# Performance work log

Measured on AMD Instinct MI355X. Metric: run time of the kernel, lower is better.

Reference implementation:

```python
import jax, jax.numpy as jnp
import numpy as np

DIM = 768
NUM_HEADS = 12
DECAY_RATE = 5.0


def setup_inputs() -> dict:
    key = jax.random.key(0)
    k1, k2, k3, k4 = jax.random.split(key, 4)
    B, N, C = 4, 1024, DIM
    x = jax.random.normal(k1, (B, N, C), dtype=jnp.float32)
    # torch nn.Linear weights: y = x @ W.T ; qkv_bias=False
    qkv_w = jax.random.normal(k2, (3 * C, C), dtype=jnp.float32) * (1.0 / np.sqrt(C))
    proj_w = jax.random.normal(k3, (C, C), dtype=jnp.float32) * (1.0 / np.sqrt(C))
    proj_b = jax.random.normal(k4, (C,), dtype=jnp.float32) * 0.01
    return {"x": x, "qkv_w": qkv_w, "proj_w": proj_w, "proj_b": proj_b, "cur_epoch": 3}


def reference(x, qkv_w, proj_w, proj_b, cur_epoch):
    B, N, C = x.shape
    H = NUM_HEADS
    hd = C // H
    scale = hd ** -0.5

    qkv = (x @ qkv_w.T).reshape(B, N, 3, H, hd).transpose(2, 0, 3, 1, 4)  # [3,B,H,N,hd]
    q, k, v = qkv[0], qkv[1], qkv[2]

    scores = jnp.einsum("bhqd,bhkd->bhqk", q, k) * scale
    logp = jax.nn.log_softmax(scores, axis=-1)
    attn = jnp.exp(logp)  # [B,H,N,N]

    # Per-key entropy: column j of attn flattened over (B,H,N) is renormalized
    # by Categorical; dividing by num_heads cancels under normalization.
    # H(p/s) = log(s) - (1/s) * sum(p * log p)
    s = jnp.sum(attn, axis=(0, 1, 2))                 # [N]
    plogp = jnp.sum(attn * logp, axis=(0, 1, 2))      # [N]
    entropies = jnp.log(s) - plogp / s

    # threshold decay: factor = sum_{i=0}^{cur_epoch-1} decay*exp(-(i+1))
    factor = DECAY_RATE * float(np.sum(np.exp(-(np.arange(cur_epoch) + 1.0))))
    entropy_threshold = float(np.log(C)) - factor

    # attn[:,:,:,keep] @ v[:,:,keep,:] == (attn * mask) @ v  (zeroed columns drop out)
    mask = (entropies <= entropy_threshold).astype(attn.dtype)  # [N]
    out = jnp.einsum("bhqk,bhkd->bhqd", attn * mask[None, None, None, :], v)
    out = out.transpose(0, 2, 1, 3).reshape(B, N, C)
    out = out @ proj_w.T + proj_b
    return out
```

## Files before the change

### kernel.cpp

```cpp
#include <hip/hip_runtime.h>


typedef __bf16 bf16x8 __attribute__((ext_vector_type(8)));
typedef __bf16 bf16x4 __attribute__((ext_vector_type(4)));
typedef float  f32x4  __attribute__((ext_vector_type(4)));

#define MFMA16(a, b, c) __builtin_amdgcn_mfma_f32_16x16x32_bf16((a), (b), (c), 0, 0, 0)

__global__ __launch_bounds__(256) void kc_conv(
    const float* __restrict__ x, const float* __restrict__ qw, const float* __restrict__ pw,
    __bf16* __restrict__ xb, __bf16* __restrict__ qwb, __bf16* __restrict__ pwb,
    float* __restrict__ colSP, int* __restrict__ keepCnt)
{
  const int i = blockIdx.x * 256 + threadIdx.x;
  const float4* src;
  __bf16* dst;
  int j;
  if (i < 786432)       { src = (const float4*)x;  dst = xb;  j = i; }
  else if (i < 1228800) { src = (const float4*)qw; dst = qwb; j = i - 786432; }
  else                  { src = (const float4*)pw; dst = pwb; j = i - 1228800; }
  const float4 f = src[j];
  bf16x4 o;
  o[0] = (__bf16)f.x; o[1] = (__bf16)f.y; o[2] = (__bf16)f.z; o[3] = (__bf16)f.w;
  *(bf16x4*)(dst + 4 * (size_t)j) = o;
  if (i < 2048) colSP[i] = 0.f;
  if (i == 0) *keepCnt = 0;
}

__global__ __launch_bounds__(256) void kg_qkv(
    const __bf16* __restrict__ A, const __bf16* __restrict__ Bm,
    __bf16* __restrict__ qb, __bf16* __restrict__ kb, float* __restrict__ v)
{
  __shared__ __bf16 As[64 * 72];
  __shared__ __bf16 Bs[64 * 72];
  const int tid = threadIdx.x;
  const int w = tid >> 6, lane = tid & 63, quad = lane >> 4, l = lane & 15;
  const int r0 = blockIdx.y * 64, c0 = blockIdx.x * 64;
  const int row = tid >> 3, ko = (tid & 7) * 8;
  const f32x4 zero = {0.f, 0.f, 0.f, 0.f};
  f32x4 acc[4];
#pragma unroll
  for (int ct = 0; ct < 4; ++ct) acc[ct] = zero;

  uint4 a0 = *(const uint4*)(A + (size_t)(r0 + row) * 768 + ko);
  uint4 a1 = *(const uint4*)(A + (size_t)(r0 + row + 32) * 768 + ko);
  uint4 b0 = *(const uint4*)(Bm + (size_t)(c0 + row) * 768 + ko);
  uint4 b1 = *(const uint4*)(Bm + (size_t)(c0 + row + 32) * 768 + ko);

  for (int k0 = 0; k0 < 768; k0 += 64) {
    __syncthreads();
    *(uint4*)&As[row * 72 + ko] = a0;
    *(uint4*)&As[(row + 32) * 72 + ko] = a1;
    *(uint4*)&Bs[row * 72 + ko] = b0;
    *(uint4*)&Bs[(row + 32) * 72 + ko] = b1;
    __syncthreads();
    if (k0 < 704) {
      a0 = *(const uint4*)(A + (size_t)(r0 + row) * 768 + k0 + 64 + ko);
      a1 = *(const uint4*)(A + (size_t)(r0 + row + 32) * 768 + k0 + 64 + ko);
      b0 = *(const uint4*)(Bm + (size_t)(c0 + row) * 768 + k0 + 64 + ko);
      b1 = *(const uint4*)(Bm + (size_t)(c0 + row + 32) * 768 + k0 + 64 + ko);
    }
    const bf16x8 af0 = *(const bf16x8*)&As[(w * 16 + l) * 72 + quad * 8];
    const bf16x8 af1 = *(const bf16x8*)&As[(w * 16 + l) * 72 + 32 + quad * 8];
#pragma unroll
    for (int ct = 0; ct < 4; ++ct) {
      const bf16x8 bf0 = *(const bf16x8*)&Bs[(ct * 16 + l) * 72 + quad * 8];
      const bf16x8 bf1 = *(const bf16x8*)&Bs[(ct * 16 + l) * 72 + 32 + quad * 8];
      acc[ct] = MFMA16(af0, bf0, acc[ct]);
      acc[ct] = MFMA16(af1, bf1, acc[ct]);
    }
  }
  const int part = c0 / 768;
  const int h = (c0 % 768) >> 6;
#pragma unroll
  for (int ct = 0; ct < 4; ++ct) {
    const int d = ct * 16 + l;
#pragma unroll
    for (int i = 0; i < 4; ++i) {
      const int rg = r0 + w * 16 + quad * 4 + i;
      const int b_ = rg >> 10, n = rg & 1023;
      const size_t off = ((size_t)(b_ * 12 + h) * 1024 + n) * 64 + d;
      const float val = acc[ct][i];
      if (part == 0)      qb[off] = (__bf16)val;
      else if (part == 1) kb[off] = (__bf16)val;
      else                v[off]  = val;
    }
  }
}

__global__ __launch_bounds__(256) void ks_fused(
    const __bf16* __restrict__ qb, const __bf16* __restrict__ kb,
    float* __restrict__ lse, float* __restrict__ partial)
{
  __shared__ __bf16 Ks[64 * 72];
  __shared__ float sS[1024];
  __shared__ float sP[1024];
  const int tid = threadIdx.x;
  const int w = tid >> 6, lane = tid & 63, quad = lane >> 4, l = lane & 15;
  const int bh = blockIdx.x, r0 = blockIdx.y * 64;
  const int row = tid >> 3, ko = (tid & 7) * 8;
  for (int i = tid; i < 1024; i += 256) { sS[i] = 0.f; sP[i] = 0.f; }

  const __bf16* qrow = qb + ((size_t)bh * 1024 + r0 + w * 16 + l) * 64;
  const bf16x8 aq0 = *(const bf16x8*)(qrow + quad * 8);
  const bf16x8 aq1 = *(const bf16x8*)(qrow + 32 + quad * 8);
  const __bf16* kbase = kb + (size_t)bh * 65536;
  const f32x4 zero = {0.f, 0.f, 0.f, 0.f};

  uint4 ka0 = *(const uint4*)(kbase + (size_t)row * 64 + ko);
  uint4 ka1 = *(const uint4*)(kbase + (size_t)(row + 32) * 64 + ko);

  float z[4] = {0.f, 0.f, 0.f, 0.f};
  for (int chunk = 0; chunk < 16; ++chunk) {
    __syncthreads();
    *(uint4*)&Ks[row * 72 + ko] = ka0;
    *(uint4*)&Ks[(row + 32) * 72 + ko] = ka1;
    __syncthreads();
    const int nxt = (chunk < 15) ? (chunk + 1) : 0;
    ka0 = *(const uint4*)(kbase + (size_t)(nxt * 64 + row) * 64 + ko);
    ka1 = *(const uint4*)(kbase + (size_t)(nxt * 64 + row + 32) * 64 + ko);
#pragma unroll
    for (int ct = 0; ct < 4; ++ct) {
      const bf16x8 kf0 = *(const bf16x8*)&Ks[(ct * 16 + l) * 72 + quad * 8];
      const bf16x8 kf1 = *(const bf16x8*)&Ks[(ct * 16 + l) * 72 + 32 + quad * 8];
      f32x4 acc = MFMA16(aq0, kf0, zero);
      acc = MFMA16(aq1, kf1, acc);
#pragma unroll
      for (int r = 0; r < 4; ++r) z[r] += __expf(acc[r] * 0.125f);
    }
  }
#pragma unroll
  for (int off = 1; off < 16; off <<= 1) {
#pragma unroll
    for (int r = 0; r < 4; ++r) z[r] += __shfl_xor(z[r], off);
  }
  float ls[4];
#pragma unroll
  for (int r = 0; r < 4; ++r) ls[r] = __logf(z[r]);
  if (l == 0) {
#pragma unroll
    for (int r = 0; r < 4; ++r)
      lse[bh * 1024 + r0 + w * 16 + quad * 4 + r] = ls[r];
  }

  for (int chunk = 0; chunk < 16; ++chunk) {
    __syncthreads();
    *(uint4*)&Ks[row * 72 + ko] = ka0;
    *(uint4*)&Ks[(row + 32) * 72 + ko] = ka1;
    __syncthreads();
    if (chunk < 15) {
      ka0 = *(const uint4*)(kbase + (size_t)((chunk + 1) * 64 + row) * 64 + ko);
      ka1 = *(const uint4*)(kbase + (size_t)((chunk + 1) * 64 + row + 32) * 64 + ko);
    }
#pragma unroll
    for (int ct = 0; ct < 4; ++ct) {
      const bf16x8 kf0 = *(const bf16x8*)&Ks[(ct * 16 + l) * 72 + quad * 8];
      const bf16x8 kf1 = *(const bf16x8*)&Ks[(ct * 16 + l) * 72 + 32 + quad * 8];
      f32x4 acc = MFMA16(aq0, kf0, zero);
      acc = MFMA16(aq1, kf1, acc);
      float sp = 0.f, spl = 0.f;
#pragma unroll
      for (int r = 0; r < 4; ++r) {
        const float lp = acc[r] * 0.125f - ls[r];
        const float p = __expf(lp);
        sp += p;
        spl += p * lp;
      }
      sp += __shfl_xor(sp, 16);   sp += __shfl_xor(sp, 32);
      spl += __shfl_xor(spl, 16); spl += __shfl_xor(spl, 32);
      if (lane < 16) {
        atomicAdd(&sS[chunk * 64 + ct * 16 + l], sp);
        atomicAdd(&sP[chunk * 64 + ct * 16 + l], spl);
      }
    }
  }
  __syncthreads();
  float* pb = partial + (size_t)(blockIdx.x * 16 + blockIdx.y) * 2048;
  for (int i = tid; i < 1024; i += 256) {
    pb[i] = sS[i];
    pb[1024 + i] = sP[i];
  }
}

__global__ __launch_bounds__(256) void kr_reduce(
    const float* __restrict__ partial, float* __restrict__ colSP)
{
  const int col = blockIdx.y * 256 + threadIdx.x;
  const float* pb = partial + (size_t)blockIdx.x * 16 * 2048 + col;
  float s = 0.f;
#pragma unroll
  for (int p = 0; p < 16; ++p) s += pb[(size_t)p * 2048];
  atomicAdd(&colSP[col], s);
}

__global__ void k_mask(const float* __restrict__ colSP, const int* __restrict__ cur_epoch,
                       float* __restrict__ mask, int* __restrict__ keepCnt)
{
  const int j = threadIdx.x;
  const float s = colSP[j];
  const float ent = __logf(s) - colSP[1024 + j] / s;
  const int ce = cur_epoch[0];
  float factor = 0.f;
  for (int i = 1; i <= ce; ++i) factor += __expf(-(float)i);
  factor *= 5.0f;
  const float thr = __logf(768.0f) - factor;
  const int keep = (ent <= thr) ? 1 : 0;
  mask[j] = keep ? 1.0f : 0.0f;
  if (keep) atomicAdd(keepCnt, 1);
}

__global__ __launch_bounds__(256) void k_av(
    const __bf16* __restrict__ qb, const __bf16* __restrict__ kb,
    const float* __restrict__ v, const float* __restrict__ lse,
    const float* __restrict__ mask, const int* __restrict__ keepCnt,
    __bf16* __restrict__ ctxb)
{
  if (*keepCnt == 0) return;
  const int tid = threadIdx.x;
  const int bh = blockIdx.x, r0 = blockIdx.y * 32;
  const int b_ = bh / 12, h = bh % 12;
  __shared__ float qs[32][64];
  __shared__ float pbuf[4][8][64];
  for (int i = tid; i < 2048; i += 256)
    qs[i >> 6][i & 63] = (float)qb[((size_t)bh * 1024 + r0) * 64 + i];
  __syncthreads();
  const int w = tid >> 6, l = tid & 63, rb = w * 8;
  float ls[8];
#pragma unroll
  for (int i = 0; i < 8; ++i) ls[i] = lse[bh * 1024 + r0 + rb + i];
  float acc[8] = {};
  for (int chunk = 0; chunk < 16; ++chunk) {
    const float mk = mask[chunk * 64 + l];
    if (__ballot(mk != 0.0f) == 0ull) continue;
    const __bf16* kp = kb + ((size_t)bh * 1024 + chunk * 64 + l) * 64;
    float s[8] = {};
    for (int d0 = 0; d0 < 64; d0 += 8) {
      const bf16x8 kf = *(const bf16x8*)(kp + d0);
#pragma unroll
      for (int dd = 0; dd < 8; ++dd) {
        const float kv = (float)kf[dd];
#pragma unroll
        for (int i = 0; i < 8; ++i) s[i] += qs[rb + i][d0 + dd] * kv;
      }
    }
    __syncthreads();
#pragma unroll
    for (int i = 0; i < 8; ++i)
      pbuf[w][i][l] = __expf(s[i] * 0.125f - ls[i]) * mk;
    __syncthreads();
    const float* vp = v + ((size_t)bh * 1024 + chunk * 64) * 64 + l;
    for (int jj = 0; jj < 64; ++jj) {
      const float vv = vp[(size_t)jj * 64];
#pragma unroll
      for (int i = 0; i < 8; ++i) acc[i] += pbuf[w][i][jj] * vv;
    }
  }
#pragma unroll
  for (int i = 0; i < 8; ++i)
    ctxb[((size_t)(b_ * 1024 + r0 + rb + i)) * 768 + h * 64 + l] = (__bf16)acc[i];
}

__global__ __launch_bounds__(256) void kg_proj(
    const __bf16* __restrict__ A, const __bf16* __restrict__ Bm,
    const float* __restrict__ bias, const int* __restrict__ keepCnt,
    float* __restrict__ out)
{
  const int tid = threadIdx.x;
  const int w = tid >> 6, lane = tid & 63, quad = lane >> 4, l = lane & 15;
  const int r0 = blockIdx.y * 64, c0 = blockIdx.x * 64;
  if (*keepCnt == 0) {
#pragma unroll
    for (int ct = 0; ct < 4; ++ct) {
      const int c = c0 + ct * 16 + l;
      const float bv = bias[c];
#pragma unroll
      for (int i = 0; i < 4; ++i) {
        const int rg = r0 + w * 16 + quad * 4 + i;
        out[(size_t)rg * 768 + c] = bv;
      }
    }
    return;
  }
  __shared__ __bf16 As[64 * 72];
  __shared__ __bf16 Bs[64 * 72];
  const int row = tid >> 3, ko = (tid & 7) * 8;
  const f32x4 zero = {0.f, 0.f, 0.f, 0.f};
  f32x4 acc[4];
#pragma unroll
  for (int ct = 0; ct < 4; ++ct) acc[ct] = zero;

  uint4 a0 = *(const uint4*)(A + (size_t)(r0 + row) * 768 + ko);
  uint4 a1 = *(const uint4*)(A + (size_t)(r0 + row + 32) * 768 + ko);
  uint4 b0 = *(const uint4*)(Bm + (size_t)(c0 + row) * 768 + ko);
  uint4 b1 = *(const uint4*)(Bm + (size_t)(c0 + row + 32) * 768 + ko);

  for (int k0 = 0; k0 < 768; k0 += 64) {
    __syncthreads();
    *(uint4*)&As[row * 72 + ko] = a0;
    *(uint4*)&As[(row + 32) * 72 + ko] = a1;
    *(uint4*)&Bs[row * 72 + ko] = b0;
    *(uint4*)&Bs[(row + 32) * 72 + ko] = b1;
    __syncthreads();
    if (k0 < 704) {
      a0 = *(const uint4*)(A + (size_t)(r0 + row) * 768 + k0 + 64 + ko);
      a1 = *(const uint4*)(A + (size_t)(r0 + row + 32) * 768 + k0 + 64 + ko);
      b0 = *(const uint4*)(Bm + (size_t)(c0 + row) * 768 + k0 + 64 + ko);
      b1 = *(const uint4*)(Bm + (size_t)(c0 + row + 32) * 768 + k0 + 64 + ko);
    }
    const bf16x8 af0 = *(const bf16x8*)&As[(w * 16 + l) * 72 + quad * 8];
    const bf16x8 af1 = *(const bf16x8*)&As[(w * 16 + l) * 72 + 32 + quad * 8];
#pragma unroll
    for (int ct = 0; ct < 4; ++ct) {
      const bf16x8 bf0 = *(const bf16x8*)&Bs[(ct * 16 + l) * 72 + quad * 8];
      const bf16x8 bf1 = *(const bf16x8*)&Bs[(ct * 16 + l) * 72 + 32 + quad * 8];
      acc[ct] = MFMA16(af0, bf0, acc[ct]);
      acc[ct] = MFMA16(af1, bf1, acc[ct]);
    }
  }
#pragma unroll
  for (int ct = 0; ct < 4; ++ct) {
    const int c = c0 + ct * 16 + l;
#pragma unroll
    for (int i = 0; i < 4; ++i) {
      const int rg = r0 + w * 16 + quad * 4 + i;
      out[(size_t)rg * 768 + c] = acc[ct][i] + bias[c];
    }
  }
}

extern "C" void kernel_launch(void* const* d_in, const int* in_sizes, int n_in,
                              void* d_out, int out_size, void* d_ws, size_t ws_size,
                              hipStream_t stream)
{
  const float* x      = (const float*)d_in[0];
  const float* qkv_w  = (const float*)d_in[1];
  const float* proj_w = (const float*)d_in[2];
  const float* proj_b = (const float*)d_in[3];
  const int*   cur_ep = (const int*)d_in[4];

  char* W = (char*)d_ws;
  __bf16* xb    = (__bf16*)(W + 0);
  __bf16* qwb   = (__bf16*)(W + 6291456);
  __bf16* pwb   = (__bf16*)(W + 9830400);
  __bf16* qb    = (__bf16*)(W + 11010048);
  __bf16* kb    = (__bf16*)(W + 17301504);
  float*  v     = (float*) (W + 23592960);
  __bf16* ctxb  = (__bf16*)(W + 36175872);
  float*  lse   = (float*) (W + 42467328);
  float*  mask  = (float*) (W + 42663936);
  int*    keep  = (int*)   (W + 42668032);
  float*  colSP = (float*) (W + 42668544);
  float*  part  = (float*) (W + 42676736);
  float*  out   = (float*)d_out;

  kc_conv<<<5376, 256, 0, stream>>>(x, qkv_w, proj_w, xb, qwb, pwb, colSP, keep);
  kg_qkv<<<dim3(36, 64), 256, 0, stream>>>(xb, qwb, qb, kb, v);
  ks_fused<<<dim3(48, 16), 256, 0, stream>>>(qb, kb, lse, part);
  kr_reduce<<<dim3(48, 8), 256, 0, stream>>>(part, colSP);
  k_mask<<<1, 1024, 0, stream>>>(colSP, cur_ep, mask, keep);
  k_av<<<dim3(48, 32), 256, 0, stream>>>(qb, kb, v, lse, mask, keep, ctxb);
  kg_proj<<<dim3(12, 64), 256, 0, stream>>>(ctxb, pwb, proj_b, keep, out);
}
```

Measured before the change: 179.9 us.

## Double query rows per block, fold partial reduction into atomics, drop reduce kernel

Each ks_fused block now covers 128 query rows (two 16-row tiles per wave), so every K tile staged in shared memory feeds twice the MFMA work. Grid size and K reloads are halved. The separate kr_reduce kernel and its partial buffer are removed; blocks atomically add their column sums straight into colSP. The exp is rewritten as exp2f with a folded log2e constant, and p*logp is algebraically restructured using precomputed 1/z and log(z)/z. The trade-offs are more register pressure, fewer blocks (384) to fill the GPU, and more global atomic contention.

```diff
diff --git a/kernel.cpp b/kernel.cpp
--- a/kernel.cpp
+++ b/kernel.cpp
@@ -6,6 +6,7 @@
 typedef float  f32x4  __attribute__((ext_vector_type(4)));
 
 #define MFMA16(a, b, c) __builtin_amdgcn_mfma_f32_16x16x32_bf16((a), (b), (c), 0, 0, 0)
+#define LOG2E_8 0.18033688f
 
 __global__ __launch_bounds__(256) void kc_conv(
     const float* __restrict__ x, const float* __restrict__ qw, const float* __restrict__ pw,
@@ -90,27 +91,31 @@
 
 __global__ __launch_bounds__(256) void ks_fused(
     const __bf16* __restrict__ qb, const __bf16* __restrict__ kb,
-    float* __restrict__ lse, float* __restrict__ partial)
+    float* __restrict__ lse, float* __restrict__ colSP)
 {
   __shared__ __bf16 Ks[64 * 72];
   __shared__ float sS[1024];
   __shared__ float sP[1024];
   const int tid = threadIdx.x;
   const int w = tid >> 6, lane = tid & 63, quad = lane >> 4, l = lane & 15;
-  const int bh = blockIdx.x, r0 = blockIdx.y * 64;
+  const int bh = blockIdx.x, r0 = blockIdx.y * 128;
   const int row = tid >> 3, ko = (tid & 7) * 8;
   for (int i = tid; i < 1024; i += 256) { sS[i] = 0.f; sP[i] = 0.f; }
 
-  const __bf16* qrow = qb + ((size_t)bh * 1024 + r0 + w * 16 + l) * 64;
-  const bf16x8 aq0 = *(const bf16x8*)(qrow + quad * 8);
-  const bf16x8 aq1 = *(const bf16x8*)(qrow + 32 + quad * 8);
+  const __bf16* qbase = qb + ((size_t)bh * 1024 + r0 + w * 32 + l) * 64;
+  bf16x8 aq0[2], aq1[2];
+#pragma unroll
+  for (int rt = 0; rt < 2; ++rt) {
+    aq0[rt] = *(const bf16x8*)(qbase + (size_t)rt * 16 * 64 + quad * 8);
+    aq1[rt] = *(const bf16x8*)(qbase + (size_t)rt * 16 * 64 + 32 + quad * 8);
+  }
   const __bf16* kbase = kb + (size_t)bh * 65536;
   const f32x4 zero = {0.f, 0.f, 0.f, 0.f};
 
   uint4 ka0 = *(const uint4*)(kbase + (size_t)row * 64 + ko);
   uint4 ka1 = *(const uint4*)(kbase + (size_t)(row + 32) * 64 + ko);
 
-  float z[4] = {0.f, 0.f, 0.f, 0.f};
+  float z[8] = {};
   for (int chunk = 0; chunk < 16; ++chunk) {
     __syncthreads();
     *(uint4*)&Ks[row * 72 + ko] = ka0;
@@ -123,24 +128,34 @@
     for (int ct = 0; ct < 4; ++ct) {
       const bf16x8 kf0 = *(const bf16x8*)&Ks[(ct * 16 + l) * 72 + quad * 8];
       const bf16x8 kf1 = *(const bf16x8*)&Ks[(ct * 16 + l) * 72 + 32 + quad * 8];
-      f32x4 acc = MFMA16(aq0, kf0, zero);
-      acc = MFMA16(aq1, kf1, acc);
-#pragma unroll
-      for (int r = 0; r < 4; ++r) z[r] += __expf(acc[r] * 0.125f);
+#pragma unroll
+      for (int rt = 0; rt < 2; ++rt) {
+        f32x4 acc = MFMA16(aq0[rt], kf0, zero);
+        acc = MFMA16(aq1[rt], kf1, acc);
+#pragma unroll
+        for (int r = 0; r < 4; ++r) z[rt * 4 + r] += exp2f(acc[r] * LOG2E_8);
+      }
     }
   }
 #pragma unroll
   for (int off = 1; off < 16; off <<= 1) {
 #pragma unroll
-    for (int r = 0; r < 4; ++r) z[r] += __shfl_xor(z[r], off);
-  }
-  float ls[4];
-#pragma unroll
-  for (int r = 0; r < 4; ++r) ls[r] = __logf(z[r]);
+    for (int i = 0; i < 8; ++i) z[i] += __shfl_xor(z[i], off);
+  }
+  float uu[8], ww[8];
+#pragma unroll
+  for (int i = 0; i < 8; ++i) {
+    const float lg = __logf(z[i]);
+    uu[i] = 1.0f / z[i];
+    ww[i] = lg * uu[i];
+    z[i] = lg;
+  }
   if (l == 0) {
 #pragma unroll
-    for (int r = 0; r < 4; ++r)
-      lse[bh * 1024 + r0 + w * 16 + quad * 4 + r] = ls[r];
+    for (int rt = 0; rt < 2; ++rt)
+#pragma unroll
+      for (int r = 0; r < 4; ++r)
+        lse[bh * 1024 + r0 + w * 32 + rt * 16 + quad * 4 + r] = z[rt * 4 + r];
   }
 
   for (int chunk = 0; chunk < 16; ++chunk) {
@@ -156,41 +171,33 @@
     for (int ct = 0; ct < 4; ++ct) {
       const bf16x8 kf0 = *(const bf16x8*)&Ks[(ct * 16 + l) * 72 + quad * 8];
       const bf16x8 kf1 = *(const bf16x8*)&Ks[(ct * 16 + l) * 72 + 32 + quad * 8];
-      f32x4 acc = MFMA16(aq0, kf0, zero);
-      acc = MFMA16(aq1, kf1, acc);
-      float sp = 0.f, spl = 0.f;
-#pragma unroll
-      for (int r = 0; r < 4; ++r) {
-        const float lp = acc[r] * 0.125f - ls[r];
-        const float p = __expf(lp);
-        sp += p;
-        spl += p * lp;
-      }
-      sp += __shfl_xor(sp, 16);   sp += __shfl_xor(sp, 32);
-      spl += __shfl_xor(spl, 16); spl += __shfl_xor(spl, 32);
+      float cs = 0.f, cp = 0.f;
+#pragma unroll
+      for (int rt = 0; rt < 2; ++rt) {
+        f32x4 acc = MFMA16(aq0[rt], kf0, zero);
+        acc = MFMA16(aq1[rt], kf1, acc);
+#pragma unroll
+        for (int r = 0; r < 4; ++r) {
+          const float sg = acc[r] * 0.125f;
+          const float e = exp2f(acc[r] * LOG2E_8);
+          const float t = e * uu[rt * 4 + r];
+          cs += t;
+          cp += t * sg - e * ww[rt * 4 + r];
+        }
+      }
+      cs += __shfl_xor(cs, 16); cs += __shfl_xor(cs, 32);
+      cp += __shfl_xor(cp, 16); cp += __shfl_xor(cp, 32);
       if (lane < 16) {
-        atomicAdd(&sS[chunk * 64 + ct * 16 + l], sp);
-        atomicAdd(&sP[chunk * 64 + ct * 16 + l], spl);
+        atomicAdd(&sS[chunk * 64 + ct * 16 + l], cs);
+        atomicAdd(&sP[chunk * 64 + ct * 16 + l], cp);
       }
     }
   }
   __syncthreads();
-  float* pb = partial + (size_t)(blockIdx.x * 16 + blockIdx.y) * 2048;
   for (int i = tid; i < 1024; i += 256) {
-    pb[i] = sS[i];
-    pb[1024 + i] = sP[i];
-  }
-}
-
-__global__ __launch_bounds__(256) void kr_reduce(
-    const float* __restrict__ partial, float* __restrict__ colSP)
-{
-  const int col = blockIdx.y * 256 + threadIdx.x;
-  const float* pb = partial + (size_t)blockIdx.x * 16 * 2048 + col;
-  float s = 0.f;
-#pragma unroll
-  for (int p = 0; p < 16; ++p) s += pb[(size_t)p * 2048];
-  atomicAdd(&colSP[col], s);
+    atomicAdd(&colSP[i], sS[i]);
+    atomicAdd(&colSP[1024 + i], sP[i]);
+  }
 }
 
 __global__ void k_mask(const float* __restrict__ colSP, const int* __restrict__ cur_epoch,
@@ -350,13 +357,11 @@
   float*  mask  = (float*) (W + 42663936);
   int*    keep  = (int*)   (W + 42668032);
   float*  colSP = (float*) (W + 42668544);
-  float*  part  = (float*) (W + 42676736);
   float*  out   = (float*)d_out;
 
   kc_conv<<<5376, 256, 0, stream>>>(x, qkv_w, proj_w, xb, qwb, pwb, colSP, keep);
   kg_qkv<<<dim3(36, 64), 256, 0, stream>>>(xb, qwb, qb, kb, v);
-  ks_fused<<<dim3(48, 16), 256, 0, stream>>>(qb, kb, lse, part);
-  kr_reduce<<<dim3(48, 8), 256, 0, stream>>>(part, colSP);
+  ks_fused<<<dim3(48, 8), 256, 0, stream>>>(qb, kb, lse, colSP);
   k_mask<<<1, 1024, 0, stream>>>(colSP, cur_ep, mask, keep);
   k_av<<<dim3(48, 32), 256, 0, stream>>>(qb, kb, v, lse, mask, keep, ctxb);
   kg_proj<<<dim3(12, 64), 256, 0, stream>>>(ctxb, pwb, proj_b, keep, out);
```

New measurement: 185.1 us. 2.9% more time.
